# Kernel tuning notes

Hardware: AMD Instinct MI355X
Metric: run time of the kernel (lower is better)

## Reference

```python
import jax, jax.numpy as jnp
import numpy as np

H = 512        # hidden_size
ENC = 2 * H    # encoder (context) feature dim
V = 10000      # vocab_size
B, T, L = 32, 500, 100
NEG_INF = -1e10


def setup_inputs() -> dict:
    key = jax.random.key(0)
    ks = jax.random.split(key, 16)
    sc = 0.02
    inp = {
        "h_batch": jax.random.normal(ks[0], (B, T, ENC), jnp.float32),
        "seq_lens": jax.random.randint(ks[1], (B,), 1, T + 1),
        "labels": jax.random.randint(ks[2], (B, L), 0, V),
        # content-based (additive) attention params
        "attn_Ws": jax.random.normal(ks[3], (H, H), jnp.float32) * sc,
        "attn_Wh": jax.random.normal(ks[4], (ENC, H), jnp.float32) * sc,
        "attn_b": jnp.zeros((H,), jnp.float32),
        "attn_v": jax.random.normal(ks[5], (H,), jnp.float32) * sc,
        # output path
        "W_sy": jax.random.normal(ks[6], (H, H), jnp.float32) * sc,
        "b_sy": jnp.zeros((H,), jnp.float32),
        "W_gy": jax.random.normal(ks[7], (ENC, H), jnp.float32) * sc,
        "b_gy": jnp.zeros((H,), jnp.float32),
        "W_yy": jax.random.normal(ks[8], (H, V), jnp.float32) * sc,
        "b_yy": jnp.zeros((V,), jnp.float32),
        # recurrence path
        "E_yr": jax.random.normal(ks[9], (V, 4 * H), jnp.float32) * sc,
        "W_sr": jax.random.normal(ks[10], (H, 4 * H), jnp.float32) * sc,
        "b_sr": jnp.zeros((4 * H,), jnp.float32),
        "W_gr": jax.random.normal(ks[11], (ENC, 4 * H), jnp.float32) * sc,
        "b_gr": jnp.zeros((4 * H,), jnp.float32),
    }
    return inp


def _func_lstm(rec_in, c):
    i, f, g, o = jnp.split(rec_in, 4, axis=-1)
    c_new = jax.nn.sigmoid(f) * c + jax.nn.sigmoid(i) * jnp.tanh(g)
    s_new = jax.nn.sigmoid(o) * jnp.tanh(c_new)
    return s_new, c_new


def reference(h_batch, seq_lens, labels, attn_Ws, attn_Wh, attn_b, attn_v,
              W_sy, b_sy, W_gy, b_gy, W_yy, b_yy,
              E_yr, W_sr, b_sr, W_gr, b_gr):
    Tlen = h_batch.shape[1]
    mask = jnp.arange(Tlen)[None, :] < seq_lens[:, None]          # [B,T]
    h_proj = jnp.einsum('bte,eh->bth', h_batch, attn_Wh) + attn_b  # precompute

    s0 = jnp.zeros((h_batch.shape[0], H), h_batch.dtype)
    c0 = jnp.zeros_like(s0)

    def step(carry, y_t):
        s, c = carry
        # content-based attention: e = v . tanh(Ws s + Wh h)
        e = jnp.einsum('bth,h->bt', jnp.tanh(h_proj + (s @ attn_Ws)[:, None, :]), attn_v)
        e = jnp.where(mask, e, NEG_INF)
        alpha = jax.nn.softmax(e, axis=-1)                         # [B,T]
        g = jnp.einsum('bt,bte->be', alpha, h_batch)               # [B,ENC]
        dec_feat = (g @ W_gy + b_gy) + (s @ W_sy + b_sy)
        y = jnp.tanh(dec_feat) @ W_yy + b_yy                       # [B,V]
        rec_in = E_yr[y_t] + (s @ W_sr + b_sr) + (g @ W_gr + b_gr) # [B,4H]
        s_new, c_new = _func_lstm(rec_in, c)
        return (s_new, c_new), y

    _, preds = jax.lax.scan(step, (s0, c0), labels.T)              # [L,B,V]
    return jnp.transpose(preds, (1, 0, 2))                         # [B,L,V]
```

## Files before the change

### kernel.cpp

```cpp
#include <hip/hip_runtime.h>
#include <cstdint>

#define B_   32
#define T_   500
#define H_   512
#define ENC_ 1024
#define V_   10000
#define L_   100
#define H4_  2048
#define NB_  256
#define NT_  512

#define OFF_HPROJ 0
#define OFF_WYYP  4096000
#define OFF_WRECP 6656000
#define OFF_WSB   10588160
#define OFF_S     10719232
#define OFF_DECTP 10735616
#define OFF_RACC  10752000
#define OFF_G0    10817536
#define OFF_G1    10850304
#define OFF_E     10883072
#define OFF_DEN   10899456
#define OFF_BAR   10899520
#define ZERO_CNT  180352

using bf16x8 = __attribute__((ext_vector_type(8))) short;
using f32x4  = __attribute__((ext_vector_type(4))) float;

__device__ __forceinline__ f32x4 mfma16(bf16x8 a, bf16x8 b, f32x4 c){
  return __builtin_amdgcn_mfma_f32_16x16x32_bf16(a, b, c, 0, 0, 0);
}
__device__ __forceinline__ unsigned short bfr(float f){
  unsigned x = __float_as_uint(f);
  return (unsigned short)((x + 0x7FFFu + ((x>>16)&1u)) >> 16);
}
__device__ __forceinline__ void bfsplit(float f, short& hi, short& lo){
  unsigned short h = bfr(f);
  float hf = __uint_as_float(((unsigned)h) << 16);
  hi = (short)h;
  lo = (short)bfr(f - hf);
}
__device__ __forceinline__ float bf2f(unsigned short u){
  return __uint_as_float(((unsigned)u) << 16);
}
__device__ __forceinline__ float ftanh(float x){
  float t = fminf(fmaxf(2.f*x, -30.f), 30.f);
  float e = __expf(t);
  return (e - 1.f) / (e + 1.f);
}
__device__ __forceinline__ float fsig(float x){
  float t = fminf(fmaxf(x, -30.f), 30.f);
  return 1.f / (1.f + __expf(-t));
}
__device__ __forceinline__ float gload(const float* p){
  return __hip_atomic_load((float*)p, __ATOMIC_RELAXED, __HIP_MEMORY_SCOPE_AGENT);
}
__device__ __forceinline__ void gstore(float* p, float v){
  __hip_atomic_store(p, v, __ATOMIC_RELAXED, __HIP_MEMORY_SCOPE_AGENT);
}
__device__ __forceinline__ void gstoreu(unsigned* p, unsigned v){
  __hip_atomic_store(p, v, __ATOMIC_RELAXED, __HIP_MEMORY_SCOPE_AGENT);
}
__device__ __forceinline__ void gload2(const float* p, float& a, float& b){
  unsigned long long u = __hip_atomic_load((const unsigned long long*)p,
                          __ATOMIC_RELAXED, __HIP_MEMORY_SCOPE_AGENT);
  a = __uint_as_float((unsigned)u);
  b = __uint_as_float((unsigned)(u >> 32));
}
__device__ __forceinline__ void gloadu2(const unsigned* p, unsigned& a, unsigned& b){
  unsigned long long u = __hip_atomic_load((const unsigned long long*)p,
                          __ATOMIC_RELAXED, __HIP_MEMORY_SCOPE_AGENT);
  a = (unsigned)u;
  b = (unsigned)(u >> 32);
}

__device__ __forceinline__ void gridbar(unsigned* bars, unsigned it){
  asm volatile("s_waitcnt vmcnt(0) lgkmcnt(0)" ::: "memory");
  __syncthreads();
  if (threadIdx.x == 0){
    unsigned* gc = bars + 1 + (blockIdx.x & 15);
    unsigned old = __hip_atomic_fetch_add(gc, 1u, __ATOMIC_RELAXED, __HIP_MEMORY_SCOPE_AGENT);
    if (old == it*16u + 15u)
      __hip_atomic_fetch_add(bars, 1u, __ATOMIC_RELAXED, __HIP_MEMORY_SCOPE_AGENT);
    while (__hip_atomic_load(bars, __ATOMIC_RELAXED, __HIP_MEMORY_SCOPE_AGENT) < (it+1u)*16u)
      __builtin_amdgcn_s_sleep(2);
  }
  __syncthreads();
  asm volatile("" ::: "memory");
}

__global__ void k_init(float* __restrict__ ws){
  int i = blockIdx.x * 256 + threadIdx.x;
  if (i < ZERO_CNT) ws[OFF_S + i] = 0.f;
}

__global__ void k_packWyy(const float* __restrict__ Wyy, float* __restrict__ ws){
  unsigned short* wp = (unsigned short*)(ws + OFF_WYYP);
  int t = blockIdx.x * 256 + threadIdx.x;
  if (t >= 625*16*64) return;
  int vt = t / 1024;
  int rem = t - vt*1024;
  int kc = rem >> 6, lane = rem & 63;
  int v  = vt*16 + (lane & 15);
  int k0 = kc*32 + ((lane >> 4) << 3);
  bf16x8 H;
  #pragma unroll
  for (int j = 0; j < 8; ++j) H[j] = (short)bfr(Wyy[(size_t)(k0+j)*V_ + v]);
  *(bf16x8*)(wp + ((size_t)(vt*16 + kc)*64 + lane)*8) = H;
}

__global__ void k_packWrec(const float* __restrict__ Wsy, const float* __restrict__ Wgy,
                           const float* __restrict__ Wsr, const float* __restrict__ Wgr,
                           float* __restrict__ ws){
  unsigned short* wp = (unsigned short*)(ws + OFF_WRECP);
  int t = blockIdx.x * 256 + threadIdx.x;
  if (t >= 160*48*64) return;
  int vt = t / (48*64);
  int rem = t - vt*(48*64);
  int kc = rem >> 6, lane = rem & 63;
  int col = vt*16 + (lane & 15);
  int k0  = kc*32 + ((lane >> 4) << 3);
  bf16x8 H, Lo;
  #pragma unroll
  for (int j = 0; j < 8; ++j){
    int k = k0 + j;
    float x;
    if (k < 512) x = (col < 512) ? Wsy[(size_t)k*512 + col] : Wsr[(size_t)k*2048 + (col-512)];
    else         x = (col < 512) ? Wgy[(size_t)(k-512)*512 + col] : Wgr[(size_t)(k-512)*2048 + (col-512)];
    short h, lo; bfsplit(x, h, lo);
    H[j] = h; Lo[j] = lo;
  }
  size_t base = ((size_t)(vt*48 + kc)*2)*512 + (size_t)lane*8;
  *(bf16x8*)(wp + base) = H;
  *(bf16x8*)(wp + base + 512) = Lo;
}

__global__ void k_packWs(const float* __restrict__ Ws, float* __restrict__ ws){
  unsigned short* wp = (unsigned short*)(ws + OFF_WSB);
  int i = blockIdx.x * 256 + threadIdx.x;
  wp[i] = bfr(Ws[i]);
}

__global__ void k_hproj(const float* __restrict__ A, const float* __restrict__ W,
                        const float* __restrict__ bias, const int* __restrict__ lens,
                        float* __restrict__ ws){
  unsigned short* C = (unsigned short*)(ws + OFF_HPROJ);
  const int bm = blockIdx.x * 64;
  const int bn = blockIdx.y * 64;
  {
    int b0 = bm / T_, t0 = bm % T_;
    int b1 = (bm + 63) / T_;
    if (b0 == b1 && t0 >= lens[b0]) return;
  }
  __shared__ float As[64][33];
  __shared__ float Bs[32][68];
  const int tid = threadIdx.x;
  const int tx = tid & 15, ty = tid >> 4;
  float acc[4][4];
  #pragma unroll
  for (int i = 0; i < 4; ++i)
    #pragma unroll
    for (int j = 0; j < 4; ++j) acc[i][j] = 0.f;
  for (int k0 = 0; k0 < 1024; k0 += 32){
    for (int i = tid; i < 64*32; i += 256){
      int rr = i >> 5, cc = i & 31;
      As[rr][cc] = A[(size_t)(bm + rr) * 1024 + k0 + cc];
    }
    for (int i = tid; i < 32*64; i += 256){
      int rr = i >> 6, cc = i & 63;
      Bs[rr][cc] = W[(size_t)(k0 + rr) * 512 + bn + cc];
    }
    __syncthreads();
    #pragma unroll
    for (int kk = 0; kk < 32; ++kk){
      float a0 = As[ty*4+0][kk], a1 = As[ty*4+1][kk];
      float a2 = As[ty*4+2][kk], a3 = As[ty*4+3][kk];
      float4 b4 = *(const float4*)&Bs[kk][tx*4];
      acc[0][0] += a0*b4.x; acc[0][1] += a0*b4.y; acc[0][2] += a0*b4.z; acc[0][3] += a0*b4.w;
      acc[1][0] += a1*b4.x; acc[1][1] += a1*b4.y; acc[1][2] += a1*b4.z; acc[1][3] += a1*b4.w;
      acc[2][0] += a2*b4.x; acc[2][1] += a2*b4.y; acc[2][2] += a2*b4.z; acc[2][3] += a2*b4.w;
      acc[3][0] += a3*b4.x; acc[3][1] += a3*b4.y; acc[3][2] += a3*b4.z; acc[3][3] += a3*b4.w;
    }
    __syncthreads();
  }
  #pragma unroll
  for (int i = 0; i < 4; ++i){
    int m = bm + ty*4 + i;
    ushort4 o;
    o.x = bfr(acc[i][0] + bias[bn + tx*4 + 0]);
    o.y = bfr(acc[i][1] + bias[bn + tx*4 + 1]);
    o.z = bfr(acc[i][2] + bias[bn + tx*4 + 2]);
    o.w = bfr(acc[i][3] + bias[bn + tx*4 + 3]);
    *(ushort4*)&C[(size_t)m * 512 + bn + tx*4] = o;
  }
}

__global__ __launch_bounds__(NT_, 2) void k_persist(
    const float* __restrict__ hb,  const int* __restrict__ lens,
    const int* __restrict__ labels, const float* __restrict__ av,
    const float* __restrict__ bsy, const float* __restrict__ bgy,
    const float* __restrict__ byy,
    const float* __restrict__ Eyr,
    const float* __restrict__ bsr, const float* __restrict__ bgr,
    float* __restrict__ out, float* __restrict__ ws)
{
  const int blk = blockIdx.x;
  const int tid = threadIdx.x;
  const int w   = tid >> 6;
  const int lane= tid & 63;
  unsigned* bars = (unsigned*)(ws + OFF_BAR);
  const unsigned short* wyyp  = (const unsigned short*)(ws + OFF_WYYP);
  const unsigned short* wrecp = (const unsigned short*)(ws + OFF_WRECP);
  const unsigned short* wsb   = (const unsigned short*)(ws + OFF_WSB);
  const unsigned short* hpB   = (const unsigned short*)(ws + OFF_HPROJ);
  unsigned* dectP = (unsigned*)(ws + OFF_DECTP);
  __shared__ __align__(16) float smem[4096];

  const int arow  = lane & 15;
  const int klane = (lane >> 4) << 3;
  float c_reg = 0.f;

  for (int l = 0; l <= L_; ++l){
    const int p = l & 1;
    const int goff = p ? OFF_G1 : OFF_G0;
    if (blk < 157){
      if (l > 0){
        const int kh = w & 1;
        const int vtslot = w >> 1;
        const int vt = blk*4 + vtslot;
        f32x4 a0 = {0.f,0.f,0.f,0.f}, a1 = {0.f,0.f,0.f,0.f};
        if (vt < 625){
          for (int kc2 = 0; kc2 < 8; ++kc2){
            const int kc = kh*8 + kc2;
            const int k0 = kc*32 + klane;
            bf16x8 Ahi0, Alo0, Ahi1, Alo1;
            {
              unsigned q[8];
              const unsigned* dp = dectP + arow*H_ + k0;
              gloadu2(dp+0, q[0], q[1]);
              gloadu2(dp+2, q[2], q[3]);
              gloadu2(dp+4, q[4], q[5]);
              gloadu2(dp+6, q[6], q[7]);
              #pragma unroll
              for (int j = 0; j < 8; ++j){
                Ahi0[j] = (short)(q[j] >> 16);
                Alo0[j] = (short)(q[j] & 0xFFFFu);
              }
            }
            {
              unsigned q[8];
              const unsigned* dp = dectP + (arow+16)*H_ + k0;
              gloadu2(dp+0, q[0], q[1]);
              gloadu2(dp+2, q[2], q[3]);
              gloadu2(dp+4, q[4], q[5]);
              gloadu2(dp+6, q[6], q[7]);
              #pragma unroll
              for (int j = 0; j < 8; ++j){
                Ahi1[j] = (short)(q[j] >> 16);
                Alo1[j] = (short)(q[j] & 0xFFFFu);
              }
            }
            bf16x8 Bv = *(const bf16x8*)(wyyp + ((size_t)(vt*16 + kc)*64 + lane)*8);
            a0 = mfma16(Ahi0, Bv, a0);
            a0 = mfma16(Alo0, Bv, a0);
            a1 = mfma16(Ahi1, Bv, a1);
            a1 = mfma16(Alo1, Bv, a1);
          }
        }
        if (vt < 625 && kh == 0){
          #pragma unroll
          for (int r = 0; r < 4; ++r){
            smem[vtslot*512 +       lane*4 + r] = a0[r];
            smem[vtslot*512 + 256 + lane*4 + r] = a1[r];
          }
        }
        __syncthreads();
        if (vt < 625 && kh == 1){
          const int v = vt*16 + arow;
          const float bv = byy[v];
          const int lv = l - 1;
          #pragma unroll
          for (int r = 0; r < 4; ++r){
            const int row0 = ((lane >> 4) << 2) + r;
            float v0 = smem[vtslot*512 +       lane*4 + r] + a0[r] + bv;
            float v1 = smem[vtslot*512 + 256 + lane*4 + r] + a1[r] + bv;
            out[((size_t)(row0)*L_      + lv)*V_ + v] = v0;
            out[((size_t)(row0 + 16)*L_ + lv)*V_ + v] = v1;
          }
        }
        __syncthreads();
      }
    } else if (blk < 221){
      if (l < L_){
        const int u = blk - 157;
        const int b = u >> 1, half = u & 1;
        float* ssm = smem;
        float* part = smem + 512;
        float* wsm = smem + 2560;
        if (l == 0){
          ssm[tid] = 0.f;
          c_reg = 0.f;
        } else {
          const int h = tid;
          const float* ey = Eyr + (size_t)labels[b*L_ + (l-1)] * H4_;
          float ri = gload(&ws[OFF_RACC + b*H4_ + h])        + bsr[h]      + bgr[h]      + ey[h];
          float rf = gload(&ws[OFF_RACC + b*H4_ + 512 + h])  + bsr[512+h]  + bgr[512+h]  + ey[512+h];
          float rg = gload(&ws[OFF_RACC + b*H4_ + 1024 + h]) + bsr[1024+h] + bgr[1024+h] + ey[1024+h];
          float ro = gload(&ws[OFF_RACC + b*H4_ + 1536 + h]) + bsr[1536+h] + bgr[1536+h] + ey[1536+h];
          float cn = fsig(rf)*c_reg + fsig(ri)*ftanh(rg);
          float sn = fsig(ro)*ftanh(cn);
          c_reg = cn;
          if (half == 0) gstore(&ws[OFF_S + b*H_ + h], sn);
          ssm[h] = sn;
        }
        __syncthreads();
        {
          const int colp = tid & 255;
          const int kh2  = tid >> 8;
          const int col0 = colp*2;
          const float* sp = ssm + kh2*256;
          const unsigned short* wb = wsb + (size_t)(kh2*256)*512 + col0;
          float acc0 = 0.f, acc1 = 0.f;
          for (int k = 0; k < 256; k += 8){
            float4 s0 = *(const float4*)&sp[k];
            float4 s1 = *(const float4*)&sp[k+4];
            unsigned wv[8];
            #pragma unroll
            for (int j = 0; j < 8; ++j)
              wv[j] = *(const unsigned*)&wb[(size_t)(k+j)*512];
            float sv[8] = {s0.x,s0.y,s0.z,s0.w,s1.x,s1.y,s1.z,s1.w};
            #pragma unroll
            for (int j = 0; j < 8; ++j){
              acc0 += sv[j] * bf2f((unsigned short)(wv[j] & 0xFFFFu));
              acc1 += sv[j] * bf2f((unsigned short)(wv[j] >> 16));
            }
          }
          part[kh2*1024 + col0]     = acc0;
          part[kh2*1024 + col0 + 1] = acc1;
        }
        __syncthreads();
        wsm[tid] = part[tid] + part[1024 + tid];
        __syncthreads();
        const int len = lens[b];
        float avr[8], swr[8];
        #pragma unroll
        for (int j = 0; j < 8; ++j){
          avr[j] = av[lane*8 + j];
          swr[j] = wsm[lane*8 + j];
        }
        float* e = ws + OFF_E;
        for (int t = 2*w + half; t < len; t += 16){
          bf16x8 hp = *(const bf16x8*)&hpB[(size_t)(b*T_ + t)*512 + lane*8];
          float sum = 0.f;
          #pragma unroll
          for (int j = 0; j < 8; ++j)
            sum += avr[j] * ftanh(bf2f((unsigned short)hp[j]) + swr[j]);
          #pragma unroll
          for (int off = 32; off > 0; off >>= 1) sum += __shfl_xor(sum, off, 64);
          if (lane == 0) gstore(&e[b*T_ + t], __expf(sum));
        }
      }
    } else {
      if (l < L_){
        for (int i = (blk - 221)*NT_ + tid; i < B_*ENC_; i += 35*NT_)
          gstore(&ws[goff + i], 0.f);
        if (blk == 221 && tid < 32)
          gstore(&ws[OFF_DEN + p*32 + tid], 0.f);
      }
    }
    if (l == L_) break;
    gridbar(bars, (unsigned)(l*3 + 0));

    {
      const int b = blk >> 3, ts = blk & 7;
      const int len = lens[b];
      const int clen = (len + 7) >> 3;
      const int t0 = ts*clen;
      const int t1 = min(t0 + clen, len);
      const int n  = t1 - t0;
      float* sc = smem;
      if (tid < n) sc[tid] = gload(&ws[OFF_E + b*T_ + t0 + tid]);
      __syncthreads();
      if (n > 0 && tid < 64){
        float s2 = 0.f;
        for (int i = tid; i < n; i += 64) s2 += sc[i];
        #pragma unroll
        for (int off = 32; off > 0; off >>= 1) s2 += __shfl_xor(s2, off, 64);
        if (tid == 0) atomicAdd(&ws[OFF_DEN + p*32 + b], s2);
      }
      if (n > 0){
        const int col0 = tid*2;
        const float* hp = hb + (size_t)b*T_*ENC_ + col0;
        float ax = 0.f, ay = 0.f;
        for (int t = t0; t < t1; ++t){
          float2 x = *(const float2*)&hp[(size_t)t * ENC_];
          float a = sc[t - t0];
          ax += a*x.x; ay += a*x.y;
        }
        float* gp = ws + goff + b*ENC_ + col0;
        atomicAdd(gp+0, ax);
        atomicAdd(gp+1, ay);
      }
    }
    gridbar(bars, (unsigned)(l*3 + 1));

    if (blk < 80){
      const float invb0 = 1.f / gload(&ws[OFF_DEN + p*32 + arow]);
      const float invb1 = 1.f / gload(&ws[OFF_DEN + p*32 + arow + 16]);
      const int sub = w >> 2;
      const int w4  = w & 3;
      const int vt  = blk*2 + sub;
      f32x4 acc0 = {0.f,0.f,0.f,0.f}, acc1 = {0.f,0.f,0.f,0.f};
      for (int c = 0; c < 3; ++c){
        #pragma unroll
        for (int kc2 = 0; kc2 < 4; ++kc2){
          const int kc = c*16 + w4*4 + kc2;
          const int k0 = kc*32 + klane;
          const bool isg = (k0 >= 512);
          bf16x8 Ahi0, Alo0, Ahi1, Alo1;
          {
            const float* src = !isg ? &ws[OFF_S + arow*H_ + k0]
                                    : &ws[goff + arow*ENC_ + (k0 - 512)];
            float x[8];
            gload2(src+0, x[0], x[1]);
            gload2(src+2, x[2], x[3]);
            gload2(src+4, x[4], x[5]);
            gload2(src+6, x[6], x[7]);
            if (isg){
              #pragma unroll
              for (int j = 0; j < 8; ++j) x[j] *= invb0;
            }
            #pragma unroll
            for (int j = 0; j < 8; ++j){
              short h, lo; bfsplit(x[j], h, lo);
              Ahi0[j] = h; Alo0[j] = lo;
            }
          }
          {
            const float* src = !isg ? &ws[OFF_S + (arow+16)*H_ + k0]
                                    : &ws[goff + (arow+16)*ENC_ + (k0 - 512)];
            float x[8];
            gload2(src+0, x[0], x[1]);
            gload2(src+2, x[2], x[3]);
            gload2(src+4, x[4], x[5]);
            gload2(src+6, x[6], x[7]);
            if (isg){
              #pragma unroll
              for (int j = 0; j < 8; ++j) x[j] *= invb1;
            }
            #pragma unroll
            for (int j = 0; j < 8; ++j){
              short h, lo; bfsplit(x[j], h, lo);
              Ahi1[j] = h; Alo1[j] = lo;
            }
          }
          const unsigned short* wp = wrecp + ((size_t)(vt*48 + kc)*2)*512 + (size_t)lane*8;
          bf16x8 Bhi = *(const bf16x8*)wp;
          bf16x8 Blo = *(const bf16x8*)(wp + 512);
          acc0 = mfma16(Ahi0, Bhi, acc0);
          acc0 = mfma16(Alo0, Bhi, acc0);
          acc0 = mfma16(Ahi0, Blo, acc0);
          acc1 = mfma16(Ahi1, Bhi, acc1);
          acc1 = mfma16(Alo1, Bhi, acc1);
          acc1 = mfma16(Ahi1, Blo, acc1);
        }
      }
      #pragma unroll
      for (int r = 0; r < 4; ++r){
        smem[sub*2048 + w4*512 +       lane*4 + r] = acc0[r];
        smem[sub*2048 + w4*512 + 256 + lane*4 + r] = acc1[r];
      }
      __syncthreads();
      #pragma unroll
      for (int oo = 0; oo < 2; ++oo){
        const int q   = tid + oo*512;
        const int sb  = q >> 9;
        const int rem = q & 511;
        const int bt  = rem >> 8;
        const int r8  = rem & 255;
        const int ln  = r8 >> 2, rr = r8 & 3;
        float v = smem[sb*2048 +        bt*256 + r8] + smem[sb*2048 +  512 + bt*256 + r8]
                + smem[sb*2048 + 1024 + bt*256 + r8] + smem[sb*2048 + 1536 + bt*256 + r8];
        const int row = bt*16 + ((ln >> 4) << 2) + rr;
        const int col = (blk*2 + sb)*16 + (ln & 15);
        if (col < 512){
          float t = ftanh(v + bsy[col] + bgy[col]);
          unsigned short hi_ = bfr(t);
          unsigned short lo_ = bfr(t - bf2f(hi_));
          gstoreu(&dectP[row*H_ + col], ((unsigned)hi_ << 16) | lo_);
        } else {
          gstore(&ws[OFF_RACC + row*H4_ + (col - 512)], v);
        }
      }
    }
    gridbar(bars, (unsigned)(l*3 + 2));
  }
}

extern "C" void kernel_launch(void* const* d_in, const int* in_sizes, int n_in,
                              void* d_out, int out_size, void* d_ws, size_t ws_size,
                              hipStream_t stream){
  const float* h_batch = (const float*)d_in[0];
  const int*   seq_lens= (const int*)d_in[1];
  const int*   labels  = (const int*)d_in[2];
  const float* attn_Ws = (const float*)d_in[3];
  const float* attn_Wh = (const float*)d_in[4];
  const float* attn_b  = (const float*)d_in[5];
  const float* attn_v  = (const float*)d_in[6];
  const float* W_sy    = (const float*)d_in[7];
  const float* b_sy    = (const float*)d_in[8];
  const float* W_gy    = (const float*)d_in[9];
  const float* b_gy    = (const float*)d_in[10];
  const float* W_yy    = (const float*)d_in[11];
  const float* b_yy    = (const float*)d_in[12];
  const float* E_yr    = (const float*)d_in[13];
  const float* W_sr    = (const float*)d_in[14];
  const float* b_sr    = (const float*)d_in[15];
  const float* W_gr    = (const float*)d_in[16];
  const float* b_gr    = (const float*)d_in[17];
  float* out = (float*)d_out;
  float* ws  = (float*)d_ws;

  k_init    <<<705, 256, 0, stream>>>(ws);
  k_packWyy <<<2500, 256, 0, stream>>>(W_yy, ws);
  k_packWrec<<<1920, 256, 0, stream>>>(W_sy, W_gy, W_sr, W_gr, ws);
  k_packWs  <<<1024, 256, 0, stream>>>(attn_Ws, ws);
  k_hproj   <<<dim3(250, 8), 256, 0, stream>>>(h_batch, attn_Wh, attn_b, seq_lens, ws);

  void* kargs[] = {
    (void*)&h_batch, (void*)&seq_lens, (void*)&labels, (void*)&attn_v,
    (void*)&b_sy, (void*)&b_gy, (void*)&b_yy,
    (void*)&E_yr, (void*)&b_sr, (void*)&b_gr,
    (void*)&out, (void*)&ws
  };
  hipLaunchCooperativeKernel((void*)k_persist, dim3(NB_), dim3(NT_), kargs, 0, stream);
}
```

Before: 10.35 ms.

## Stream bf16 copy of h_batch for context sum and re-split recurrence GEMM warps

A new pre-pass converts h_batch to bf16 in the workspace. The persistent kernel's context-vector accumulation now reads this bf16 copy with 4-wide loads, splits timesteps across two thread groups, and reduces the halves through shared memory before the atomics. This halves the bytes streamed per step, at the cost of bf16 rounding in the attention context. The recurrence GEMM phase also changes its warp split: each of the 8 warps now covers a 6-chunk K slice for both column tiles, with an 8-way shared-memory reduction replacing the earlier 4-way one.

```diff
diff --git a/kernel.cpp b/kernel.cpp
--- a/kernel.cpp
+++ b/kernel.cpp
@@ -23,6 +23,7 @@
 #define OFF_E     10883072
 #define OFF_DEN   10899456
 #define OFF_BAR   10899520
+#define OFF_HB16  10899584
 #define ZERO_CNT  180352
 
 using bf16x8 = __attribute__((ext_vector_type(8))) short;
@@ -140,6 +141,12 @@
   unsigned short* wp = (unsigned short*)(ws + OFF_WSB);
   int i = blockIdx.x * 256 + threadIdx.x;
   wp[i] = bfr(Ws[i]);
+}
+
+__global__ void k_packHB(const float* __restrict__ hb, float* __restrict__ ws){
+  unsigned short* wp = (unsigned short*)(ws + OFF_HB16);
+  int i = blockIdx.x * 256 + threadIdx.x;
+  if (i < B_*T_*ENC_) wp[i] = bfr(hb[i]);
 }
 
 __global__ void k_hproj(const float* __restrict__ A, const float* __restrict__ W,
@@ -197,7 +204,7 @@
 }
 
 __global__ __launch_bounds__(NT_, 2) void k_persist(
-    const float* __restrict__ hb,  const int* __restrict__ lens,
+    const int* __restrict__ lens,
     const int* __restrict__ labels, const float* __restrict__ av,
     const float* __restrict__ bsy, const float* __restrict__ bgy,
     const float* __restrict__ byy,
@@ -214,8 +221,9 @@
   const unsigned short* wrecp = (const unsigned short*)(ws + OFF_WRECP);
   const unsigned short* wsb   = (const unsigned short*)(ws + OFF_WSB);
   const unsigned short* hpB   = (const unsigned short*)(ws + OFF_HPROJ);
+  const unsigned short* hb16  = (const unsigned short*)(ws + OFF_HB16);
   unsigned* dectP = (unsigned*)(ws + OFF_DECTP);
-  __shared__ __align__(16) float smem[4096];
+  __shared__ __align__(16) float smem[8192];
 
   const int arow  = lane & 15;
   const int klane = (lane >> 4) << 3;
@@ -380,6 +388,7 @@
       const int t1 = min(t0 + clen, len);
       const int n  = t1 - t0;
       float* sc = smem;
+      float* pg = smem + 128;
       if (tid < n) sc[tid] = gload(&ws[OFF_E + b*T_ + t0 + tid]);
       __syncthreads();
       if (n > 0 && tid < 64){
@@ -389,18 +398,28 @@
         for (int off = 32; off > 0; off >>= 1) s2 += __shfl_xor(s2, off, 64);
         if (tid == 0) atomicAdd(&ws[OFF_DEN + p*32 + b], s2);
       }
-      if (n > 0){
-        const int col0 = tid*2;
-        const float* hp = hb + (size_t)b*T_*ENC_ + col0;
-        float ax = 0.f, ay = 0.f;
-        for (int t = t0; t < t1; ++t){
-          float2 x = *(const float2*)&hp[(size_t)t * ENC_];
+      const int tg = tid >> 8, cq = tid & 255;
+      const int col0 = cq*4;
+      {
+        float4 acc = {0.f,0.f,0.f,0.f};
+        const unsigned short* hp = hb16 + (size_t)b*T_*ENC_ + col0;
+        for (int t = t0 + tg; t < t1; t += 2){
+          ushort4 x = *(const ushort4*)&hp[(size_t)t * ENC_];
           float a = sc[t - t0];
-          ax += a*x.x; ay += a*x.y;
-        }
+          acc.x += a*bf2f(x.x); acc.y += a*bf2f(x.y);
+          acc.z += a*bf2f(x.z); acc.w += a*bf2f(x.w);
+        }
+        *(float4*)&pg[tg*1024 + col0] = acc;
+      }
+      __syncthreads();
+      if (tg == 0 && n > 0){
+        float4 x0 = *(const float4*)&pg[col0];
+        float4 x1 = *(const float4*)&pg[1024 + col0];
         float* gp = ws + goff + b*ENC_ + col0;
-        atomicAdd(gp+0, ax);
-        atomicAdd(gp+1, ay);
+        atomicAdd(gp+0, x0.x+x1.x);
+        atomicAdd(gp+1, x0.y+x1.y);
+        atomicAdd(gp+2, x0.z+x1.z);
+        atomicAdd(gp+3, x0.w+x1.w);
       }
     }
     gridbar(bars, (unsigned)(l*3 + 1));
@@ -408,82 +427,88 @@
     if (blk < 80){
       const float invb0 = 1.f / gload(&ws[OFF_DEN + p*32 + arow]);
       const float invb1 = 1.f / gload(&ws[OFF_DEN + p*32 + arow + 16]);
-      const int sub = w >> 2;
-      const int w4  = w & 3;
-      const int vt  = blk*2 + sub;
-      f32x4 acc0 = {0.f,0.f,0.f,0.f}, acc1 = {0.f,0.f,0.f,0.f};
-      for (int c = 0; c < 3; ++c){
+      f32x4 acc[2][2];
+      #pragma unroll
+      for (int vv = 0; vv < 2; ++vv)
         #pragma unroll
-        for (int kc2 = 0; kc2 < 4; ++kc2){
-          const int kc = c*16 + w4*4 + kc2;
-          const int k0 = kc*32 + klane;
-          const bool isg = (k0 >= 512);
-          bf16x8 Ahi0, Alo0, Ahi1, Alo1;
-          {
-            const float* src = !isg ? &ws[OFF_S + arow*H_ + k0]
-                                    : &ws[goff + arow*ENC_ + (k0 - 512)];
-            float x[8];
-            gload2(src+0, x[0], x[1]);
-            gload2(src+2, x[2], x[3]);
-            gload2(src+4, x[4], x[5]);
-            gload2(src+6, x[6], x[7]);
-            if (isg){
-              #pragma unroll
-              for (int j = 0; j < 8; ++j) x[j] *= invb0;
-            }
+        for (int rg = 0; rg < 2; ++rg) acc[vv][rg] = (f32x4){0.f,0.f,0.f,0.f};
+      for (int j6 = 0; j6 < 6; ++j6){
+        const int kc = w*6 + j6;
+        const int k0 = kc*32 + klane;
+        const bool isg = (k0 >= 512);
+        bf16x8 Ahi0, Alo0, Ahi1, Alo1;
+        {
+          const float* src = !isg ? &ws[OFF_S + arow*H_ + k0]
+                                  : &ws[goff + arow*ENC_ + (k0 - 512)];
+          float x[8];
+          gload2(src+0, x[0], x[1]);
+          gload2(src+2, x[2], x[3]);
+          gload2(src+4, x[4], x[5]);
+          gload2(src+6, x[6], x[7]);
+          if (isg){
             #pragma unroll
-            for (int j = 0; j < 8; ++j){
-              short h, lo; bfsplit(x[j], h, lo);
-              Ahi0[j] = h; Alo0[j] = lo;
-            }
-          }
-          {
-            const float* src = !isg ? &ws[OFF_S + (arow+16)*H_ + k0]
-                                    : &ws[goff + (arow+16)*ENC_ + (k0 - 512)];
-            float x[8];
-            gload2(src+0, x[0], x[1]);
-            gload2(src+2, x[2], x[3]);
-            gload2(src+4, x[4], x[5]);
-            gload2(src+6, x[6], x[7]);
-            if (isg){
-              #pragma unroll
-              for (int j = 0; j < 8; ++j) x[j] *= invb1;
-            }
+            for (int j = 0; j < 8; ++j) x[j] *= invb0;
+          }
+          #pragma unroll
+          for (int j = 0; j < 8; ++j){
+            short h, lo; bfsplit(x[j], h, lo);
+            Ahi0[j] = h; Alo0[j] = lo;
+          }
+        }
+        {
+          const float* src = !isg ? &ws[OFF_S + (arow+16)*H_ + k0]
+                                  : &ws[goff + (arow+16)*ENC_ + (k0 - 512)];
+          float x[8];
+          gload2(src+0, x[0], x[1]);
+          gload2(src+2, x[2], x[3]);
+          gload2(src+4, x[4], x[5]);
+          gload2(src+6, x[6], x[7]);
+          if (isg){
             #pragma unroll
-            for (int j = 0; j < 8; ++j){
-              short h, lo; bfsplit(x[j], h, lo);
-              Ahi1[j] = h; Alo1[j] = lo;
-            }
-          }
+            for (int j = 0; j < 8; ++j) x[j] *= invb1;
+          }
+          #pragma unroll
+          for (int j = 0; j < 8; ++j){
+            short h, lo; bfsplit(x[j], h, lo);
+            Ahi1[j] = h; Alo1[j] = lo;
+          }
+        }
+        #pragma unroll
+        for (int vv = 0; vv < 2; ++vv){
+          const int vt = blk*2 + vv;
           const unsigned short* wp = wrecp + ((size_t)(vt*48 + kc)*2)*512 + (size_t)lane*8;
           bf16x8 Bhi = *(const bf16x8*)wp;
           bf16x8 Blo = *(const bf16x8*)(wp + 512);
-          acc0 = mfma16(Ahi0, Bhi, acc0);
-          acc0 = mfma16(Alo0, Bhi, acc0);
-          acc0 = mfma16(Ahi0, Blo, acc0);
-          acc1 = mfma16(Ahi1, Bhi, acc1);
-          acc1 = mfma16(Alo1, Bhi, acc1);
-          acc1 = mfma16(Ahi1, Blo, acc1);
+          acc[vv][0] = mfma16(Ahi0, Bhi, acc[vv][0]);
+          acc[vv][0] = mfma16(Alo0, Bhi, acc[vv][0]);
+          acc[vv][0] = mfma16(Ahi0, Blo, acc[vv][0]);
+          acc[vv][1] = mfma16(Ahi1, Bhi, acc[vv][1]);
+          acc[vv][1] = mfma16(Alo1, Bhi, acc[vv][1]);
+          acc[vv][1] = mfma16(Ahi1, Blo, acc[vv][1]);
         }
       }
       #pragma unroll
-      for (int r = 0; r < 4; ++r){
-        smem[sub*2048 + w4*512 +       lane*4 + r] = acc0[r];
-        smem[sub*2048 + w4*512 + 256 + lane*4 + r] = acc1[r];
-      }
+      for (int vv = 0; vv < 2; ++vv)
+        #pragma unroll
+        for (int rg = 0; rg < 2; ++rg)
+          #pragma unroll
+          for (int r = 0; r < 4; ++r)
+            smem[((w*2 + vv)*2 + rg)*256 + lane*4 + r] = acc[vv][rg][r];
       __syncthreads();
       #pragma unroll
       for (int oo = 0; oo < 2; ++oo){
         const int q   = tid + oo*512;
-        const int sb  = q >> 9;
+        const int vv  = q >> 9;
         const int rem = q & 511;
         const int bt  = rem >> 8;
         const int r8  = rem & 255;
-        const int ln  = r8 >> 2, rr = r8 & 3;
-        float v = smem[sb*2048 +        bt*256 + r8] + smem[sb*2048 +  512 + bt*256 + r8]
-                + smem[sb*2048 + 1024 + bt*256 + r8] + smem[sb*2048 + 1536 + bt*256 + r8];
+        float v = 0.f;
+        #pragma unroll
+        for (int w8 = 0; w8 < 8; ++w8)
+          v += smem[((w8*2 + vv)*2 + bt)*256 + r8];
+        const int ln = r8 >> 2, rr = r8 & 3;
         const int row = bt*16 + ((ln >> 4) << 2) + rr;
-        const int col = (blk*2 + sb)*16 + (ln & 15);
+        const int col = (blk*2 + vv)*16 + (ln & 15);
         if (col < 512){
           float t = ftanh(v + bsy[col] + bgy[col]);
           unsigned short hi_ = bfr(t);
@@ -526,10 +551,11 @@
   k_packWyy <<<2500, 256, 0, stream>>>(W_yy, ws);
   k_packWrec<<<1920, 256, 0, stream>>>(W_sy, W_gy, W_sr, W_gr, ws);
   k_packWs  <<<1024, 256, 0, stream>>>(attn_Ws, ws);
+  k_packHB  <<<64000, 256, 0, stream>>>(h_batch, ws);
   k_hproj   <<<dim3(250, 8), 256, 0, stream>>>(h_batch, attn_Wh, attn_b, seq_lens, ws);
 
   void* kargs[] = {
-    (void*)&h_batch, (void*)&seq_lens, (void*)&labels, (void*)&attn_v,
+    (void*)&seq_lens, (void*)&labels, (void*)&attn_v,
     (void*)&b_sy, (void*)&b_gy, (void*)&b_yy,
     (void*)&E_yr, (void*)&b_sr, (void*)&b_gr,
     (void*)&out, (void*)&ws
```

Measured after the change: 9.609 ms. -7.1%, faster.
